# Kernel optimization log

Hardware: AMD Instinct MI355X
Metric: run time of the kernel (lower is better)

Reference implementation:

```python
import jax, jax.numpy as jnp
import numpy as np

N_NODES = 50000
N_EDGES = 800000
IN_DIM = 128
HID = 256
BN_EPS = 1e-5
NEG_SLOPE = 0.01


def setup_inputs() -> dict:
    key = jax.random.key(0)
    ks = jax.random.split(key, 8)
    inp = {
        "x": jax.random.normal(ks[0], (N_NODES, IN_DIM), dtype=jnp.float32),
        "src": jax.random.randint(ks[1], (N_EDGES,), 0, N_NODES, dtype=jnp.int32),
        "dst": jax.random.randint(ks[2], (N_EDGES,), 0, N_NODES, dtype=jnp.int32),
        # layer 0 MLP (in->hid->hid) + BN params
        "w1_0": jax.random.normal(ks[3], (IN_DIM, HID), dtype=jnp.float32) / np.sqrt(IN_DIM),
        "b1_0": jnp.zeros((HID,), jnp.float32),
        "w2_0": jax.random.normal(ks[4], (HID, HID), dtype=jnp.float32) / np.sqrt(HID),
        "b2_0": jnp.zeros((HID,), jnp.float32),
        "g0": jnp.ones((HID,), jnp.float32),
        "be0": jnp.zeros((HID,), jnp.float32),
        "m0": jnp.zeros((HID,), jnp.float32),
        "v0": jnp.ones((HID,), jnp.float32),
        # layers 1..2 stacked (hid->hid->hid) + BN params
        "w1_r": jax.random.normal(ks[5], (2, HID, HID), dtype=jnp.float32) / np.sqrt(HID),
        "b1_r": jnp.zeros((2, HID), jnp.float32),
        "w2_r": jax.random.normal(ks[6], (2, HID, HID), dtype=jnp.float32) / np.sqrt(HID),
        "b2_r": jnp.zeros((2, HID), jnp.float32),
        "g_r": jnp.ones((2, HID), jnp.float32),
        "be_r": jnp.zeros((2, HID), jnp.float32),
        "m_r": jnp.zeros((2, HID), jnp.float32),
        "v_r": jnp.ones((2, HID), jnp.float32),
    }
    return inp


def _gin_layer(h, src, dst, w1, b1, w2, b2, g, be, m, v, last):
    # GINConv (eps=0): (1+eps)*h + sum_{j in N(i)} h_j  via gather + scatter-add
    agg = jax.ops.segment_sum(h[src], dst, num_segments=N_NODES)
    z = h + agg
    # 2-layer MLP (dropout is identity in eval)
    z = jax.nn.leaky_relu(z @ w1 + b1, NEG_SLOPE)
    z = z @ w2 + b2
    # BatchNorm1d (eval: running stats)
    z = (z - m) * jax.lax.rsqrt(v + BN_EPS) * g + be
    if not last:
        z = jax.nn.leaky_relu(z, NEG_SLOPE)
    return z


def reference(x, src, dst, w1_0, b1_0, w2_0, b2_0, g0, be0, m0, v0,
              w1_r, b1_r, w2_r, b2_r, g_r, be_r, m_r, v_r):
    h = _gin_layer(x, src, dst, w1_0, b1_0, w2_0, b2_0, g0, be0, m0, v0, last=False)
    for l in range(2):
        h = _gin_layer(h, src, dst, w1_r[l], b1_r[l], w2_r[l], b2_r[l],
                       g_r[l], be_r[l], m_r[l], v_r[l], last=(l == 1))
    return h
```

## Files before the change

### kernel.cpp

```cpp
#include <hip/hip_runtime.h>
#include <hip/hip_bf16.h>
#include <stdint.h>

#define NN 50000
#define NE 800000
#define IND 128
#define HID 256
#define MPAD 50048
#define NBLK 49

#define NCH 64
#define CHSZ 12500
#define NRG 8
#define RGSZ 6250

typedef unsigned int uint32;
typedef unsigned short ushort_t;
typedef __attribute__((ext_vector_type(8))) short short8;
typedef __attribute__((ext_vector_type(4))) float f32x4;

__device__ __forceinline__ ushort_t f2b(float f) {
  uint32 u = __float_as_uint(f);
  u = (u + 0x7fffu + ((u >> 16) & 1u)) >> 16;
  return (ushort_t)u;
}
__device__ __forceinline__ float blo(uint32 u) { return __uint_as_float(u << 16); }
__device__ __forceinline__ float bhi(uint32 u) { return __uint_as_float(u & 0xffff0000u); }
__device__ __forceinline__ uint32 pack2(float a, float b) {
  return (uint32)f2b(a) | ((uint32)f2b(b) << 16);
}

__device__ __forceinline__ int packidx(int col, int k, int Kd) {
  int lane = ((k & 31) >> 3) * 16 + (col & 15);
  int c = (((col >> 6) * (Kd >> 5) + (k >> 5)) * 4 + ((col >> 4) & 3)) * 64 + lane;
  return c * 8 + (k & 7);
}

__global__ __launch_bounds__(256) void histp_k(const int* __restrict__ dst,
                                               uint32* __restrict__ partial,
                                               int* __restrict__ rnk) {
  __shared__ uint32 lh[RGSZ];
  const int c = blockIdx.x & (NCH - 1);
  const int rg = blockIdx.x >> 6;
  const int r0 = rg * RGSZ;
  for (int i = threadIdx.x; i < RGSZ; i += 256) lh[i] = 0;
  __syncthreads();
  const int e0 = c * CHSZ;
  for (int i = threadIdx.x; i < CHSZ; i += 256) {
    int e = e0 + i;
    int d = dst[e] - r0;
    if ((unsigned)d < (unsigned)RGSZ) rnk[e] = (int)atomicAdd(&lh[d], 1u);
  }
  __syncthreads();
  uint32* po = partial + (size_t)c * NN + r0;
  for (int i = threadIdx.x; i < RGSZ; i += 256) po[i] = lh[i];
}

__global__ void coff_k(uint32* __restrict__ partial, int* __restrict__ cnt) {
  int bin = blockIdx.x * 256 + threadIdx.x;
  if (bin >= NN) return;
  uint32 run = 0;
#pragma unroll
  for (int c = 0; c < NCH; c++) {
    uint32 t = partial[(size_t)c * NN + bin];
    partial[(size_t)c * NN + bin] = run;
    run += t;
  }
  cnt[bin] = (int)run;
}

__global__ void bsum_k(const int* __restrict__ cnt, int* __restrict__ bsum) {
  __shared__ int ws[16];
  const int tid = threadIdx.x, ln = tid & 63, wv = tid >> 6;
  int i = blockIdx.x * 1024 + tid;
  int v = (i < NN) ? cnt[i] : 0;
#pragma unroll
  for (int d = 32; d; d >>= 1) v += __shfl_down(v, d, 64);
  if (ln == 0) ws[wv] = v;
  __syncthreads();
  if (tid < 16) {
    int s = ws[tid];
#pragma unroll
    for (int d = 8; d; d >>= 1) s += __shfl_down(s, d, 64);
    if (tid == 0) bsum[blockIdx.x] = s;
  }
}

__global__ void bscan_k(int* __restrict__ bsum, int* __restrict__ rp) {
  int tid = threadIdx.x;
  int v = (tid < NBLK) ? bsum[tid] : 0;
  int x = v;
#pragma unroll
  for (int d = 1; d < 64; d <<= 1) {
    int t = __shfl_up(x, d, 64);
    if (tid >= d) x += t;
  }
  if (tid < NBLK) bsum[tid] = x - v;
  if (tid == 0) rp[NN] = NE;
}

__global__ void scan2_k(const int* __restrict__ cnt, const int* __restrict__ bsum,
                        int* __restrict__ rp) {
  __shared__ int ws[16];
  const int tid = threadIdx.x, ln = tid & 63, wv = tid >> 6;
  int i = blockIdx.x * 1024 + tid;
  int v = (i < NN) ? cnt[i] : 0;
  int x = v;
#pragma unroll
  for (int d = 1; d < 64; d <<= 1) {
    int t = __shfl_up(x, d, 64);
    if (ln >= d) x += t;
  }
  if (ln == 63) ws[wv] = x;
  __syncthreads();
  if (tid < 16) {
    int s = ws[tid];
#pragma unroll
    for (int d = 1; d < 16; d <<= 1) {
      int t = __shfl_up(s, d, 64);
      if (tid >= d) s += t;
    }
    ws[tid] = s;
  }
  __syncthreads();
  int excl = x - v + (wv ? ws[wv - 1] : 0) + bsum[blockIdx.x];
  if (i < NN) rp[i] = excl;
}

__global__ void scat2_k(const int* __restrict__ src, const int* __restrict__ dst,
                        const int* __restrict__ rp, const uint32* __restrict__ partial,
                        const int* __restrict__ rnk, int* __restrict__ esrc) {
  int e = blockIdx.x * 256 + threadIdx.x;
  if (e < NE) {
    int d = dst[e];
    int c = e / CHSZ;
    int pos = rp[d] + (int)partial[(size_t)c * NN + d] + rnk[e];
    esrc[pos] = src[e];
  }
}

__global__ void prep_k(const float* __restrict__ w1_0, const float* __restrict__ w2_0,
                       const float* __restrict__ w1_r, const float* __restrict__ w2_r,
                       const float* b1_0, const float* b2_0, const float* g0,
                       const float* be0, const float* m0, const float* v0,
                       const float* b1_r, const float* b2_r, const float* g_r,
                       const float* be_r, const float* m_r, const float* v_r,
                       ushort_t* __restrict__ wt,
                       float* bi1, float* sc2, float* bi2) {
  const int which = blockIdx.y;
  if (which < 6) {
    const int n = blockIdx.x, k = threadIdx.x;
    const float* w; ushort_t* o; int K = HID;
    switch (which) {
      case 0: w = w1_0; o = wt; K = IND; break;
      case 1: w = w2_0; o = wt + HID * IND; break;
      case 2: w = w1_r; o = wt + HID * IND + 1 * HID * HID; break;
      case 3: w = w2_r; o = wt + HID * IND + 2 * HID * HID; break;
      case 4: w = w1_r + HID * HID; o = wt + HID * IND + 3 * HID * HID; break;
      default: w = w2_r + HID * HID; o = wt + HID * IND + 4 * HID * HID; break;
    }
    if (k < K) o[packidx(n, k, K)] = f2b(w[(size_t)k * HID + n]);
  } else {
    const int l = blockIdx.x;
    if (l >= 3) return;
    const int j = threadIdx.x;
    float b1, b2, g, be, m, v;
    if (l == 0) { b1 = b1_0[j]; b2 = b2_0[j]; g = g0[j]; be = be0[j]; m = m0[j]; v = v0[j]; }
    else { int o = (l - 1) * HID + j; b1 = b1_r[o]; b2 = b2_r[o]; g = g_r[o]; be = be_r[o]; m = m_r[o]; v = v_r[o]; }
    int o = l * HID + j;
    bi1[o] = b1;
    float s = g * rsqrtf(v + 1e-5f);
    sc2[o] = s;
    bi2[o] = (b2 - m) * s + be;
  }
}

__global__ void x2b_k(const float* __restrict__ x, ushort_t* __restrict__ xb) {
  int i = blockIdx.x * 256 + threadIdx.x;
  const int n = NN * IND / 2;
  if (i < n) {
    float2 f = ((const float2*)x)[i];
    ((uint32*)xb)[i] = pack2(f.x, f.y);
  }
}

__global__ void agg256_k(const ushort_t* __restrict__ h, const int* __restrict__ rp,
                         const int* __restrict__ esrc, ushort_t* __restrict__ z) {
  int wid = threadIdx.x >> 6, lane = threadIdx.x & 63;
  int node = blockIdx.x * 4 + wid;
  if (node >= NN) return;
  const uint2* hp = (const uint2*)h;
  uint2 v = hp[(size_t)node * 64 + lane];
  float a0 = blo(v.x), a1 = bhi(v.x), a2 = blo(v.y), a3 = bhi(v.y);
  int e0 = rp[node], e1 = rp[node + 1];
  int e = e0;
  for (; e + 8 <= e1; e += 8) {
    int s[8];
#pragma unroll
    for (int q = 0; q < 8; q++) s[q] = esrc[e + q];
    uint2 u[8];
#pragma unroll
    for (int q = 0; q < 8; q++) u[q] = hp[(size_t)s[q] * 64 + lane];
#pragma unroll
    for (int q = 0; q < 8; q++) {
      a0 += blo(u[q].x); a1 += bhi(u[q].x); a2 += blo(u[q].y); a3 += bhi(u[q].y);
    }
  }
  for (; e < e1; e++) {
    int s = esrc[e];
    uint2 u = hp[(size_t)s * 64 + lane];
    a0 += blo(u.x); a1 += bhi(u.x); a2 += blo(u.y); a3 += bhi(u.y);
  }
  uint2 o; o.x = pack2(a0, a1); o.y = pack2(a2, a3);
  ((uint2*)z)[(size_t)node * 64 + lane] = o;
}

__global__ void agg128_k(const ushort_t* __restrict__ h, const int* __restrict__ rp,
                         const int* __restrict__ esrc, ushort_t* __restrict__ z) {
  int wid = threadIdx.x >> 6, lane = threadIdx.x & 63;
  int node = blockIdx.x * 4 + wid;
  if (node >= NN) return;
  const uint32* hp = (const uint32*)h;
  uint32 v = hp[(size_t)node * 64 + lane];
  float a0 = blo(v), a1 = bhi(v);
  int e0 = rp[node], e1 = rp[node + 1];
  int e = e0;
  for (; e + 8 <= e1; e += 8) {
    int s[8];
#pragma unroll
    for (int q = 0; q < 8; q++) s[q] = esrc[e + q];
    uint32 u[8];
#pragma unroll
    for (int q = 0; q < 8; q++) u[q] = hp[(size_t)s[q] * 64 + lane];
#pragma unroll
    for (int q = 0; q < 8; q++) { a0 += blo(u[q]); a1 += bhi(u[q]); }
  }
  for (; e < e1; e++) {
    int s = esrc[e];
    uint32 u = hp[(size_t)s * 64 + lane];
    a0 += blo(u); a1 += bhi(u);
  }
  ((uint32*)z)[(size_t)node * 64 + lane] = pack2(a0, a1);
}

template<int K1>
__global__ __launch_bounds__(256, 2) void fgemm_k(
    const ushort_t* __restrict__ A, const ushort_t* __restrict__ B1t,
    const ushort_t* __restrict__ B2t, const float* __restrict__ bi1,
    const float* __restrict__ sc2, const float* __restrict__ bi2,
    void* __restrict__ out, int lrelu2, int f32out) {
  __shared__ ushort_t C1s[64 * 264];
  const int tid = threadIdx.x;
  const int lane = tid & 63;
  const int wid = tid >> 6;
  const int m0 = blockIdx.x * 64;
  const int fr = lane & 15;
  const int fk = (lane >> 4) * 8;
  const int er = lane >> 4;
  const int ec = lane & 15;
  constexpr int S1 = K1 / 32;

  const short8* Bp1 = (const short8*)B1t;
  const short8* Bp2 = (const short8*)B2t;

  f32x4 zero = {0.f, 0.f, 0.f, 0.f};
  f32x4 acc[4][4];
#pragma unroll
  for (int i = 0; i < 4; i++)
#pragma unroll
    for (int j = 0; j < 4; j++) acc[i][j] = zero;

#pragma unroll 2
  for (int ks = 0; ks < S1; ks++) {
    const int kk = ks * 32;
    short8 af[4], bfv[4];
#pragma unroll
    for (int i = 0; i < 4; i++)
      af[i] = *(const short8*)(A + (size_t)(m0 + i * 16 + fr) * K1 + kk + fk);
#pragma unroll
    for (int j = 0; j < 4; j++)
      bfv[j] = Bp1[((wid * S1 + ks) * 4 + j) * 64 + lane];
#pragma unroll
    for (int i = 0; i < 4; i++)
#pragma unroll
      for (int j = 0; j < 4; j++)
        acc[i][j] = __builtin_amdgcn_mfma_f32_16x16x32_bf16(af[i], bfv[j], acc[i][j], 0, 0, 0);
  }

#pragma unroll
  for (int j = 0; j < 4; j++) {
    int col = wid * 64 + j * 16 + ec;
    float b = bi1[col];
#pragma unroll
    for (int i = 0; i < 4; i++) {
#pragma unroll
      for (int r = 0; r < 4; r++) {
        int row = i * 16 + er * 4 + r;
        float v = acc[i][j][r] + b;
        v = (v > 0.f) ? v : 0.01f * v;
        C1s[row * 264 + col] = f2b(v);
      }
    }
  }
  __syncthreads();

  f32x4 acc2[4][4];
#pragma unroll
  for (int i = 0; i < 4; i++)
#pragma unroll
    for (int j = 0; j < 4; j++) acc2[i][j] = zero;

#pragma unroll 2
  for (int ks = 0; ks < 8; ks++) {
    const int kk = ks * 32;
    short8 af[4], bfv[4];
#pragma unroll
    for (int i = 0; i < 4; i++)
      af[i] = *(const short8*)(C1s + (i * 16 + fr) * 264 + kk + fk);
#pragma unroll
    for (int j = 0; j < 4; j++)
      bfv[j] = Bp2[((wid * 8 + ks) * 4 + j) * 64 + lane];
#pragma unroll
    for (int i = 0; i < 4; i++)
#pragma unroll
      for (int j = 0; j < 4; j++)
        acc2[i][j] = __builtin_amdgcn_mfma_f32_16x16x32_bf16(af[i], bfv[j], acc2[i][j], 0, 0, 0);
  }

#pragma unroll
  for (int j = 0; j < 4; j++) {
    int col = wid * 64 + j * 16 + ec;
    float s = sc2[col], b = bi2[col];
#pragma unroll
    for (int i = 0; i < 4; i++) {
#pragma unroll
      for (int r = 0; r < 4; r++) {
        int row = m0 + i * 16 + er * 4 + r;
        float v = acc2[i][j][r] * s + b;
        if (lrelu2) v = (v > 0.f) ? v : 0.01f * v;
        if (row < NN) {
          if (f32out) ((float*)out)[(size_t)row * HID + col] = v;
          else        ((ushort_t*)out)[(size_t)row * HID + col] = f2b(v);
        }
      }
    }
  }
}

extern "C" void kernel_launch(void* const* d_in, const int* in_sizes, int n_in,
                              void* d_out, int out_size, void* d_ws, size_t ws_size,
                              hipStream_t stream) {
  const float* x    = (const float*)d_in[0];
  const int*   src  = (const int*)d_in[1];
  const int*   dst  = (const int*)d_in[2];
  const float* w1_0 = (const float*)d_in[3];
  const float* b1_0 = (const float*)d_in[4];
  const float* w2_0 = (const float*)d_in[5];
  const float* b2_0 = (const float*)d_in[6];
  const float* g0   = (const float*)d_in[7];
  const float* be0  = (const float*)d_in[8];
  const float* m0   = (const float*)d_in[9];
  const float* v0   = (const float*)d_in[10];
  const float* w1_r = (const float*)d_in[11];
  const float* b1_r = (const float*)d_in[12];
  const float* w2_r = (const float*)d_in[13];
  const float* b2_r = (const float*)d_in[14];
  const float* g_r  = (const float*)d_in[15];
  const float* be_r = (const float*)d_in[16];
  const float* m_r  = (const float*)d_in[17];
  const float* v_r  = (const float*)d_in[18];

  char* ws = (char*)d_ws;
  size_t off = 0;
  auto alloc = [&](size_t bytes) {
    void* p = ws + off;
    off = (off + bytes + 255) & ~(size_t)255;
    return p;
  };
  ushort_t* bufA  = (ushort_t*)alloc((size_t)MPAD * HID * 2);
  ushort_t* bufB  = (ushort_t*)alloc((size_t)MPAD * HID * 2);
  ushort_t* xb    = (ushort_t*)alloc((size_t)MPAD * IND * 2);
  int*      rp    = (int*)alloc((NN + 1) * sizeof(int));
  int*      cnt   = (int*)alloc(NN * sizeof(int));
  int*      bsum  = (int*)alloc(NBLK * sizeof(int));
  int*      esrc  = (int*)alloc((size_t)NE * sizeof(int));
  ushort_t* wt    = (ushort_t*)alloc(((size_t)HID * IND + 5 * (size_t)HID * HID) * 2);
  float*    bi1   = (float*)alloc(3 * HID * sizeof(float));
  float*    sc2   = (float*)alloc(3 * HID * sizeof(float));
  float*    bi2   = (float*)alloc(3 * HID * sizeof(float));
  (void)ws_size; (void)in_sizes; (void)n_in; (void)out_size;

  uint32* partial = (uint32*)bufA;
  int*    rnk     = (int*)bufB;

  ushort_t* w1_0t = wt;
  ushort_t* w2_0t = wt + HID * IND;
  ushort_t* w1r0t = wt + HID * IND + 1 * HID * HID;
  ushort_t* w2r0t = wt + HID * IND + 2 * HID * HID;
  ushort_t* w1r1t = wt + HID * IND + 3 * HID * HID;
  ushort_t* w2r1t = wt + HID * IND + 4 * HID * HID;

  histp_k<<<NCH * NRG, 256, 0, stream>>>(dst, partial, rnk);
  coff_k<<<(NN + 255) / 256, 256, 0, stream>>>(partial, cnt);
  bsum_k<<<NBLK, 1024, 0, stream>>>(cnt, bsum);
  bscan_k<<<1, 64, 0, stream>>>(bsum, rp);
  scan2_k<<<NBLK, 1024, 0, stream>>>(cnt, bsum, rp);
  scat2_k<<<(NE + 255) / 256, 256, 0, stream>>>(src, dst, rp, partial, rnk, esrc);

  prep_k<<<dim3(HID, 7), 256, 0, stream>>>(w1_0, w2_0, w1_r, w2_r,
                                           b1_0, b2_0, g0, be0, m0, v0,
                                           b1_r, b2_r, g_r, be_r, m_r, v_r,
                                           wt, bi1, sc2, bi2);
  x2b_k<<<(NN * IND / 2 + 255) / 256, 256, 0, stream>>>(x, xb);

  const int GG = MPAD / 64;
  agg128_k<<<NN / 4, 256, 0, stream>>>(xb, rp, esrc, bufA);
  fgemm_k<IND><<<GG, 256, 0, stream>>>(bufA, w1_0t, w2_0t, bi1, sc2, bi2, bufB, 1, 0);
  agg256_k<<<NN / 4, 256, 0, stream>>>(bufB, rp, esrc, bufA);
  fgemm_k<HID><<<GG, 256, 0, stream>>>(bufA, w1r0t, w2r0t, bi1 + HID, sc2 + HID, bi2 + HID, bufB, 1, 0);
  agg256_k<<<NN / 4, 256, 0, stream>>>(bufB, rp, esrc, bufA);
  fgemm_k<HID><<<GG, 256, 0, stream>>>(bufA, w1r1t, w2r1t, bi1 + 2 * HID, sc2 + 2 * HID, bi2 + 2 * HID, d_out, 0, 1);
}
```

Measured before the change: 433.4 us.

## Restructure CSR build: recompute ranks in scatter, single-block scan, raise GEMM occupancy

The CSR construction stops storing per-edge ranks in the histogram pass. A new scatter kernel mirrors the histogram's chunk and range tiling, recomputing ranks with LDS atomics and writing esrc directly from a per-bin base. The three-kernel prefix scan becomes one 1024-thread single-block scan, with each thread serially handling 49 bins. Separately, fgemm launch bounds go from 2 to 3 blocks per CU, which trades register budget for occupancy. The goal is fewer launches and less global traffic, at the cost of re-reading dst in every range block, a serial single-block scan, and possible register spills in the GEMM.

```diff
diff --git a/kernel.cpp b/kernel.cpp
--- a/kernel.cpp
+++ b/kernel.cpp
@@ -37,8 +37,7 @@
 }
 
 __global__ __launch_bounds__(256) void histp_k(const int* __restrict__ dst,
-                                               uint32* __restrict__ partial,
-                                               int* __restrict__ rnk) {
+                                               uint32* __restrict__ partial) {
   __shared__ uint32 lh[RGSZ];
   const int c = blockIdx.x & (NCH - 1);
   const int rg = blockIdx.x >> 6;
@@ -47,9 +46,8 @@
   __syncthreads();
   const int e0 = c * CHSZ;
   for (int i = threadIdx.x; i < CHSZ; i += 256) {
-    int e = e0 + i;
-    int d = dst[e] - r0;
-    if ((unsigned)d < (unsigned)RGSZ) rnk[e] = (int)atomicAdd(&lh[d], 1u);
+    int d = dst[e0 + i] - r0;
+    if ((unsigned)d < (unsigned)RGSZ) atomicAdd(&lh[d], 1u);
   }
   __syncthreads();
   uint32* po = partial + (size_t)c * NN + r0;
@@ -69,73 +67,71 @@
   cnt[bin] = (int)run;
 }
 
-__global__ void bsum_k(const int* __restrict__ cnt, int* __restrict__ bsum) {
-  __shared__ int ws[16];
+__global__ __launch_bounds__(1024) void scan1_k(const int* __restrict__ cnt,
+                                                int* __restrict__ rp) {
+  __shared__ int wsum[16];
   const int tid = threadIdx.x, ln = tid & 63, wv = tid >> 6;
-  int i = blockIdx.x * 1024 + tid;
-  int v = (i < NN) ? cnt[i] : 0;
-#pragma unroll
-  for (int d = 32; d; d >>= 1) v += __shfl_down(v, d, 64);
-  if (ln == 0) ws[wv] = v;
-  __syncthreads();
-  if (tid < 16) {
-    int s = ws[tid];
-#pragma unroll
-    for (int d = 8; d; d >>= 1) s += __shfl_down(s, d, 64);
-    if (tid == 0) bsum[blockIdx.x] = s;
-  }
-}
-
-__global__ void bscan_k(int* __restrict__ bsum, int* __restrict__ rp) {
-  int tid = threadIdx.x;
-  int v = (tid < NBLK) ? bsum[tid] : 0;
-  int x = v;
-#pragma unroll
-  for (int d = 1; d < 64; d <<= 1) {
-    int t = __shfl_up(x, d, 64);
-    if (tid >= d) x += t;
-  }
-  if (tid < NBLK) bsum[tid] = x - v;
-  if (tid == 0) rp[NN] = NE;
-}
-
-__global__ void scan2_k(const int* __restrict__ cnt, const int* __restrict__ bsum,
-                        int* __restrict__ rp) {
-  __shared__ int ws[16];
-  const int tid = threadIdx.x, ln = tid & 63, wv = tid >> 6;
-  int i = blockIdx.x * 1024 + tid;
-  int v = (i < NN) ? cnt[i] : 0;
-  int x = v;
+  const int b0 = tid * 49;
+  int s = 0;
+  for (int q = 0; q < 49; q++) {
+    int b = b0 + q;
+    if (b < NN) s += cnt[b];
+  }
+  int x = s;
 #pragma unroll
   for (int d = 1; d < 64; d <<= 1) {
     int t = __shfl_up(x, d, 64);
     if (ln >= d) x += t;
   }
-  if (ln == 63) ws[wv] = x;
+  if (ln == 63) wsum[wv] = x;
   __syncthreads();
   if (tid < 16) {
-    int s = ws[tid];
+    int t = wsum[tid];
+    int y = t;
 #pragma unroll
     for (int d = 1; d < 16; d <<= 1) {
-      int t = __shfl_up(s, d, 64);
-      if (tid >= d) s += t;
-    }
-    ws[tid] = s;
-  }
-  __syncthreads();
-  int excl = x - v + (wv ? ws[wv - 1] : 0) + bsum[blockIdx.x];
-  if (i < NN) rp[i] = excl;
-}
-
-__global__ void scat2_k(const int* __restrict__ src, const int* __restrict__ dst,
-                        const int* __restrict__ rp, const uint32* __restrict__ partial,
-                        const int* __restrict__ rnk, int* __restrict__ esrc) {
-  int e = blockIdx.x * 256 + threadIdx.x;
-  if (e < NE) {
-    int d = dst[e];
-    int c = e / CHSZ;
-    int pos = rp[d] + (int)partial[(size_t)c * NN + d] + rnk[e];
-    esrc[pos] = src[e];
+      int u = __shfl_up(y, d, 64);
+      if (tid >= d) y += u;
+    }
+    wsum[tid] = y - t;
+  }
+  __syncthreads();
+  int run = (x - s) + wsum[wv];
+  for (int q = 0; q < 49; q++) {
+    int b = b0 + q;
+    if (b < NN) {
+      rp[b] = run;
+      run += cnt[b];
+    }
+  }
+  if (tid == 0) rp[NN] = NE;
+}
+
+__global__ __launch_bounds__(256) void scat3_k(const int* __restrict__ src,
+                                               const int* __restrict__ dst,
+                                               const int* __restrict__ rp,
+                                               const uint32* __restrict__ partial,
+                                               int* __restrict__ esrc) {
+  __shared__ int base[RGSZ];
+  __shared__ uint32 lh[RGSZ];
+  const int c = blockIdx.x & (NCH - 1);
+  const int rg = blockIdx.x >> 6;
+  const int r0 = rg * RGSZ;
+  const uint32* po = partial + (size_t)c * NN + r0;
+  const int* rpo = rp + r0;
+  for (int i = threadIdx.x; i < RGSZ; i += 256) {
+    base[i] = rpo[i] + (int)po[i];
+    lh[i] = 0;
+  }
+  __syncthreads();
+  const int e0 = c * CHSZ;
+  for (int i = threadIdx.x; i < CHSZ; i += 256) {
+    int e = e0 + i;
+    int d = dst[e] - r0;
+    if ((unsigned)d < (unsigned)RGSZ) {
+      int r = (int)atomicAdd(&lh[d], 1u);
+      esrc[base[d] + r] = src[e];
+    }
   }
 }
 
@@ -244,7 +240,7 @@
 }
 
 template<int K1>
-__global__ __launch_bounds__(256, 2) void fgemm_k(
+__global__ __launch_bounds__(256, 3) void fgemm_k(
     const ushort_t* __restrict__ A, const ushort_t* __restrict__ B1t,
     const ushort_t* __restrict__ B2t, const float* __restrict__ bi1,
     const float* __restrict__ sc2, const float* __restrict__ bi2,
@@ -382,7 +378,6 @@
   ushort_t* xb    = (ushort_t*)alloc((size_t)MPAD * IND * 2);
   int*      rp    = (int*)alloc((NN + 1) * sizeof(int));
   int*      cnt   = (int*)alloc(NN * sizeof(int));
-  int*      bsum  = (int*)alloc(NBLK * sizeof(int));
   int*      esrc  = (int*)alloc((size_t)NE * sizeof(int));
   ushort_t* wt    = (ushort_t*)alloc(((size_t)HID * IND + 5 * (size_t)HID * HID) * 2);
   float*    bi1   = (float*)alloc(3 * HID * sizeof(float));
@@ -391,7 +386,6 @@
   (void)ws_size; (void)in_sizes; (void)n_in; (void)out_size;
 
   uint32* partial = (uint32*)bufA;
-  int*    rnk     = (int*)bufB;
 
   ushort_t* w1_0t = wt;
   ushort_t* w2_0t = wt + HID * IND;
@@ -400,12 +394,10 @@
   ushort_t* w1r1t = wt + HID * IND + 3 * HID * HID;
   ushort_t* w2r1t = wt + HID * IND + 4 * HID * HID;
 
-  histp_k<<<NCH * NRG, 256, 0, stream>>>(dst, partial, rnk);
+  histp_k<<<NCH * NRG, 256, 0, stream>>>(dst, partial);
   coff_k<<<(NN + 255) / 256, 256, 0, stream>>>(partial, cnt);
-  bsum_k<<<NBLK, 1024, 0, stream>>>(cnt, bsum);
-  bscan_k<<<1, 64, 0, stream>>>(bsum, rp);
-  scan2_k<<<NBLK, 1024, 0, stream>>>(cnt, bsum, rp);
-  scat2_k<<<(NE + 255) / 256, 256, 0, stream>>>(src, dst, rp, partial, rnk, esrc);
+  scan1_k<<<1, 1024, 0, stream>>>(cnt, rp);
+  scat3_k<<<NCH * NRG, 256, 0, stream>>>(src, dst, rp, partial, esrc);
 
   prep_k<<<dim3(HID, 7), 256, 0, stream>>>(w1_0, w2_0, w1_r, w2_r,
                                            b1_0, b2_0, g0, be0, m0, v0,
```

Result: slower. 525.1 us (+21.2%).

## Recompute edge ranks in LDS during scatter, drop rank buffer; raise fgemm occupancy

Applied to the files above, without the earlier changes.

The CSR build no longer writes a per-edge rank array in the histogram pass. A new scatter kernel uses the same chunk×range-group blocking, rebuilds the local counters in LDS, and derives each edge's slot from shared atomics plus a precomputed base. This removes the rank write and read traffic and the global partial lookup per edge, at the cost of rereading dst per range group. The order of edges within a segment becomes nondeterministic, which can perturb float sums slightly. Separately, fgemm launch bounds go from 2 to 3 blocks per CU, which may cause register spills.

```diff
diff --git a/kernel.cpp b/kernel.cpp
--- a/kernel.cpp
+++ b/kernel.cpp
@@ -37,8 +37,7 @@
 }
 
 __global__ __launch_bounds__(256) void histp_k(const int* __restrict__ dst,
-                                               uint32* __restrict__ partial,
-                                               int* __restrict__ rnk) {
+                                               uint32* __restrict__ partial) {
   __shared__ uint32 lh[RGSZ];
   const int c = blockIdx.x & (NCH - 1);
   const int rg = blockIdx.x >> 6;
@@ -47,9 +46,8 @@
   __syncthreads();
   const int e0 = c * CHSZ;
   for (int i = threadIdx.x; i < CHSZ; i += 256) {
-    int e = e0 + i;
-    int d = dst[e] - r0;
-    if ((unsigned)d < (unsigned)RGSZ) rnk[e] = (int)atomicAdd(&lh[d], 1u);
+    int d = dst[e0 + i] - r0;
+    if ((unsigned)d < (unsigned)RGSZ) atomicAdd(&lh[d], 1u);
   }
   __syncthreads();
   uint32* po = partial + (size_t)c * NN + r0;
@@ -127,15 +125,31 @@
   if (i < NN) rp[i] = excl;
 }
 
-__global__ void scat2_k(const int* __restrict__ src, const int* __restrict__ dst,
-                        const int* __restrict__ rp, const uint32* __restrict__ partial,
-                        const int* __restrict__ rnk, int* __restrict__ esrc) {
-  int e = blockIdx.x * 256 + threadIdx.x;
-  if (e < NE) {
-    int d = dst[e];
-    int c = e / CHSZ;
-    int pos = rp[d] + (int)partial[(size_t)c * NN + d] + rnk[e];
-    esrc[pos] = src[e];
+__global__ __launch_bounds__(256) void scat3_k(const int* __restrict__ src,
+                                               const int* __restrict__ dst,
+                                               const int* __restrict__ rp,
+                                               const uint32* __restrict__ partial,
+                                               int* __restrict__ esrc) {
+  __shared__ int base[RGSZ];
+  __shared__ uint32 lh[RGSZ];
+  const int c = blockIdx.x & (NCH - 1);
+  const int rg = blockIdx.x >> 6;
+  const int r0 = rg * RGSZ;
+  const uint32* po = partial + (size_t)c * NN + r0;
+  const int* rpo = rp + r0;
+  for (int i = threadIdx.x; i < RGSZ; i += 256) {
+    base[i] = rpo[i] + (int)po[i];
+    lh[i] = 0;
+  }
+  __syncthreads();
+  const int e0 = c * CHSZ;
+  for (int i = threadIdx.x; i < CHSZ; i += 256) {
+    int e = e0 + i;
+    int d = dst[e] - r0;
+    if ((unsigned)d < (unsigned)RGSZ) {
+      int r = (int)atomicAdd(&lh[d], 1u);
+      esrc[base[d] + r] = src[e];
+    }
   }
 }
 
@@ -244,7 +258,7 @@
 }
 
 template<int K1>
-__global__ __launch_bounds__(256, 2) void fgemm_k(
+__global__ __launch_bounds__(256, 3) void fgemm_k(
     const ushort_t* __restrict__ A, const ushort_t* __restrict__ B1t,
     const ushort_t* __restrict__ B2t, const float* __restrict__ bi1,
     const float* __restrict__ sc2, const float* __restrict__ bi2,
@@ -391,7 +405,6 @@
   (void)ws_size; (void)in_sizes; (void)n_in; (void)out_size;
 
   uint32* partial = (uint32*)bufA;
-  int*    rnk     = (int*)bufB;
 
   ushort_t* w1_0t = wt;
   ushort_t* w2_0t = wt + HID * IND;
@@ -400,12 +413,12 @@
   ushort_t* w1r1t = wt + HID * IND + 3 * HID * HID;
   ushort_t* w2r1t = wt + HID * IND + 4 * HID * HID;
 
-  histp_k<<<NCH * NRG, 256, 0, stream>>>(dst, partial, rnk);
+  histp_k<<<NCH * NRG, 256, 0, stream>>>(dst, partial);
   coff_k<<<(NN + 255) / 256, 256, 0, stream>>>(partial, cnt);
   bsum_k<<<NBLK, 1024, 0, stream>>>(cnt, bsum);
   bscan_k<<<1, 64, 0, stream>>>(bsum, rp);
   scan2_k<<<NBLK, 1024, 0, stream>>>(cnt, bsum, rp);
-  scat2_k<<<(NE + 255) / 256, 256, 0, stream>>>(src, dst, rp, partial, rnk, esrc);
+  scat3_k<<<NCH * NRG, 256, 0, stream>>>(src, dst, rp, partial, esrc);
 
   prep_k<<<dim3(HID, 7), 256, 0, stream>>>(w1_0, w2_0, w1_r, w2_r,
                                            b1_0, b2_0, g0, be0, m0, v0,
```

Measured after the change: 443.2 us. +2.3%, slower.
